# Optimization experiments

Measured on AMD Instinct MI355X. Metric: run time of the kernel, lower is better.

Reference implementation:

```python
import jax, jax.numpy as jnp
import numpy as np

B, S, H, F, E, K = 8, 4096, 256, 512, 16, 2
EPS = 1e-5


def setup_inputs() -> dict:
    key = jax.random.key(0)
    ks = jax.random.split(key, 9)
    sc = 0.02
    return {
        "x": jax.random.normal(ks[0], (B, S, H), dtype=jnp.float32),
        "gate_w": jax.random.normal(ks[1], (H, E), dtype=jnp.float32) * sc,
        "gate_b": jnp.zeros((E,), dtype=jnp.float32),
        "w1": jax.random.normal(ks[2], (E, H, F), dtype=jnp.float32) * sc,
        "b1": jnp.zeros((E, F), dtype=jnp.float32),
        "w2": jax.random.normal(ks[3], (E, F, H), dtype=jnp.float32) * sc,
        "b2": jnp.zeros((E, H), dtype=jnp.float32),
        "gamma": jnp.ones((H,), dtype=jnp.float32),
        "beta": jnp.zeros((H,), dtype=jnp.float32),
    }


def reference(x, gate_w, gate_b, w1, b1, w2, b2, gamma, beta):
    # gating: top-k over expert logits, softmax over the k selected logits
    gate_logits = x @ gate_w + gate_b                      # [B,S,E]
    topk_vals, topk_idx = jax.lax.top_k(gate_logits, K)    # [B,S,K]
    topk_w = jax.nn.softmax(topk_vals, axis=-1)            # [B,S,K]

    # naive dense MoE: every expert runs over every token (matches source)
    h = jax.nn.relu(jnp.einsum('bsh,ehf->bsef', x, w1) + b1)   # [B,S,E,F]
    expert_out = jnp.einsum('bsef,efh->bseh', h, w2) + b2       # [B,S,E,H]

    # select top-k expert outputs and combine with gate weights
    sel = jnp.take_along_axis(expert_out, topk_idx[:, :, :, None], axis=2)  # [B,S,K,H]
    moe = jnp.sum(topk_w[..., None] * sel, axis=2)              # [B,S,H]

    # residual + LayerNorm
    y = x + moe
    mu = jnp.mean(y, axis=-1, keepdims=True)
    var = jnp.var(y, axis=-1, keepdims=True)
    return (y - mu) / jnp.sqrt(var + EPS) * gamma + beta
```

## Files before the change

### kernel.cpp

```cpp
#include <hip/hip_runtime.h>
#include <hip/hip_bf16.h>

typedef __bf16 bf16_t;
typedef __bf16 bf16x8 __attribute__((ext_vector_type(8)));
typedef __bf16 bf16x4 __attribute__((ext_vector_type(4)));
typedef float f32x4 __attribute__((ext_vector_type(4)));

#define NB 8
#define NS 4096
#define NH 256
#define NF 512
#define NE 16
#define NTOK (NB*NS)
#define TT 64
#define NCH 16
#define HS_STRIDE 40

__device__ __forceinline__ void load_lds16(const void* g, void* l) {
    __builtin_amdgcn_global_load_lds(
        (const __attribute__((address_space(1))) unsigned int*)g,
        (__attribute__((address_space(3))) unsigned int*)l, 16, 0, 0);
}

__global__ __launch_bounds__(256) void prep_kernel(
    const float* __restrict__ w1, const float* __restrict__ w2,
    bf16_t* __restrict__ w1t, bf16_t* __restrict__ w2t,
    const float* __restrict__ x, const float* __restrict__ gate_w,
    const float* __restrict__ gate_b,
    int* __restrict__ counts, int* __restrict__ bucket_enc,
    float* __restrict__ bucket_gw, bf16_t* __restrict__ xb)
{
    __shared__ float tile[32][33];
    __shared__ int lcnt[NE];
    __shared__ int gbase[NE];

    if (blockIdx.x < 128) {
        if (threadIdx.x < NE) lcnt[threadIdx.x] = 0;
        __syncthreads();

        int tok = blockIdx.x * 256 + threadIdx.x;
        const float4* xr = (const float4*)(x + (size_t)tok * NH);
        bf16x4* xbr = (bf16x4*)(xb + (size_t)tok * NH);
        float acc[NE];
        #pragma unroll
        for (int e = 0; e < NE; e++) acc[e] = gate_b[e];
        for (int h4 = 0; h4 < NH / 4; h4++) {
            float4 xv = xr[h4];
            bf16x4 xo;
            xo[0] = (bf16_t)xv.x; xo[1] = (bf16_t)xv.y;
            xo[2] = (bf16_t)xv.z; xo[3] = (bf16_t)xv.w;
            xbr[h4] = xo;
            #pragma unroll
            for (int j = 0; j < 4; j++) {
                float xs = (j == 0) ? xv.x : (j == 1) ? xv.y : (j == 2) ? xv.z : xv.w;
                const float* wr = gate_w + (h4 * 4 + j) * NE;
                #pragma unroll
                for (int e = 0; e < NE; e++) acc[e] += xs * wr[e];
            }
        }
        float v0 = -1e30f, v1 = -1e30f; int i0 = 0, i1 = 0;
        #pragma unroll
        for (int e = 0; e < NE; e++) {
            float a = acc[e];
            if (a > v0)      { v1 = v0; i1 = i0; v0 = a; i0 = e; }
            else if (a > v1) { v1 = a; i1 = e; }
        }
        float e1 = __expf(v1 - v0);
        float s  = 1.f + e1;
        int   pe[2] = { i0, i1 };
        float pg[2] = { 1.f / s, e1 / s };
        int   po[2];
        po[0] = atomicAdd(&lcnt[i0], 1);
        po[1] = atomicAdd(&lcnt[i1], 1);
        __syncthreads();
        if (threadIdx.x < NE)
            gbase[threadIdx.x] = atomicAdd(&counts[threadIdx.x], lcnt[threadIdx.x]);
        __syncthreads();
        #pragma unroll
        for (int k = 0; k < 2; k++) {
            int e = pe[k];
            int pos = gbase[e] + po[k];
            bucket_enc[e * NTOK + pos] = tok | (k << 20);
            bucket_gw [e * NTOK + pos] = pg[k];
        }
        return;
    }

    int bid = blockIdx.x - 128;
    const float* src; bf16_t* dst; int R, C; int isw1;
    if (bid < 2048) { src = w1; dst = w1t; R = NH; C = NF; isw1 = 1; }
    else            { bid -= 2048; src = w2; dst = w2t; R = NF; C = NH; isw1 = 0; }
    int e = bid >> 7;
    int t = bid & 127;
    int tcols = C / 32;
    int tr = (t / tcols) * 32, tc = (t % tcols) * 32;
    src += (size_t)e * R * C;
    dst += (size_t)e * R * C;
    int tx = threadIdx.x & 31, ty0 = threadIdx.x >> 5;
    #pragma unroll
    for (int i = 0; i < 4; i++) {
        int ty = ty0 + i * 8;
        tile[ty][tx] = src[(size_t)(tr + ty) * C + tc + tx];
    }
    __syncthreads();
    if (threadIdx.x < 128) {
        int j = threadIdx.x & 31;
        int g = threadIdx.x >> 5;
        bf16x8 v;
        #pragma unroll
        for (int jj = 0; jj < 8; jj++)
            v[jj] = (bf16_t)tile[g * 8 + jj][j];
        size_t idx;
        if (isw1) {
            int f  = tc + j;
            int kb = tr + g * 8;
            idx = (size_t)f * NH + ((((kb >> 3) ^ (f & 7))) << 3);
        } else {
            int h  = tc + j;
            int fb = tr + g * 8;
            idx = ((size_t)(fb >> 5) * NH + h) * 32 + (fb & 31);
        }
        *(bf16x8*)(dst + idx) = v;
    }
}

__global__ __launch_bounds__(256, 3) void moe_kernel(
    const bf16_t* __restrict__ xb,
    const bf16_t* __restrict__ w1t,
    const float*  __restrict__ b1,
    const bf16_t* __restrict__ w2t,
    const float*  __restrict__ b2,
    const int* __restrict__ counts,
    const int* __restrict__ bucket_enc,
    const float* __restrict__ bucket_gw,
    bf16_t* __restrict__ pairbuf)
{
    __shared__ uint4 W1s4[2][1024];
    __shared__ __align__(16) bf16_t Hs[2][TT][HS_STRIDE];
    __shared__ int   tok_s[TT];
    __shared__ float gw_s[TT];
    __shared__ float b1_s[NF];
    __shared__ float b2_s[NH];

    int flat = blockIdx.x;
    int xcd  = flat & 7;
    int j    = flat >> 3;
    int e    = xcd * 2 + (j & 1);
    int tile0 = j >> 1;
    int n_e = counts[e];
    int wave = threadIdx.x >> 6;
    int lane = threadIdx.x & 63;
    int l15 = lane & 15, q = lane >> 4;

    const bf16_t* w1te = w1t + (size_t)e * NF * NH;
    const bf16_t* w2te = w2t + (size_t)e * NF * NH;

    if (threadIdx.x < 256) {
        b1_s[threadIdx.x]       = b1[e * NF + threadIdx.x];
        b1_s[threadIdx.x + 256] = b1[e * NF + threadIdx.x + 256];
        b2_s[threadIdx.x]       = b2[e * NH + threadIdx.x];
    }

    int ntiles = (n_e + TT - 1) / TT;
    for (int tile = tile0; tile < ntiles; tile += 48) {
        int tstart = tile * TT;
        __syncthreads();
        if (threadIdx.x < TT) {
            int slot = tstart + threadIdx.x;
            if (slot < n_e) {
                tok_s[threadIdx.x] = bucket_enc[e * NTOK + slot];
                gw_s [threadIdx.x] = bucket_gw [e * NTOK + slot];
            } else { tok_s[threadIdx.x] = 0; gw_s[threadIdx.x] = 0.f; }
        }
        __syncthreads();

        {
            const uint4* gw1 = (const uint4*)w1te;
            #pragma unroll
            for (int i = 0; i < 4; i++)
                load_lds16(gw1 + i * 256 + threadIdx.x, &W1s4[0][i * 256 + threadIdx.x]);
        }
        int mytok = tok_s[wave * 16 + l15] & 0xFFFFF;
        const uint4* xrow = (const uint4*)(xb + (size_t)mytok * NH);
        uint4 xf[8];
        #pragma unroll
        for (int ks = 0; ks < 8; ks++) xf[ks] = xrow[ks * 4 + q];
        bf16x8 bf2c[4], bf2n[4];
        #pragma unroll
        for (int nt = 0; nt < 4; nt++) {
            int hh = wave * 64 + nt * 16 + l15;
            bf2c[nt] = *(const bf16x8*)&w2te[((size_t)hh << 5) + q * 8];
        }
        __syncthreads();

        f32x4 oacc[4][4];
        #pragma unroll
        for (int a = 0; a < 4; a++)
            #pragma unroll
            for (int b = 0; b < 4; b++) { f32x4 z = {0.f,0.f,0.f,0.f}; oacc[a][b] = z; }

        for (int ch = 0; ch < NCH; ch++) {
            int buf = ch & 1;
            if (ch + 1 < NCH) {
                const uint4* gw1 = (const uint4*)w1te + (size_t)(ch + 1) * 1024;
                #pragma unroll
                for (int i = 0; i < 4; i++)
                    load_lds16(gw1 + i * 256 + threadIdx.x,
                               &W1s4[buf ^ 1][i * 256 + threadIdx.x]);
                #pragma unroll
                for (int nt = 0; nt < 4; nt++) {
                    int hh = wave * 64 + nt * 16 + l15;
                    bf2n[nt] = *(const bf16x8*)&w2te[(((size_t)(ch + 1) * NH + hh) << 5) + q * 8];
                }
                asm volatile("s_waitcnt vmcnt(12)" ::: "memory");
            } else {
                asm volatile("s_waitcnt vmcnt(4)" ::: "memory");
            }
            __builtin_amdgcn_s_barrier();
            __builtin_amdgcn_sched_barrier(0);

            f32x4 hacc[2]; { f32x4 z = {0.f,0.f,0.f,0.f}; hacc[0] = z; hacc[1] = z; }
            const bf16_t* w1s = (const bf16_t*)W1s4[buf];
            #pragma unroll
            for (int ks = 0; ks < 8; ks++) {
                bf16x8 xfrag = *(const bf16x8*)&xf[ks];
                #pragma unroll
                for (int n = 0; n < 2; n++) {
                    int fl = n * 16 + l15;
                    bf16x8 wf = *(const bf16x8*)&w1s[fl * NH + ((((ks * 4 + q) ^ (fl & 7))) << 3)];
                    hacc[n] = __builtin_amdgcn_mfma_f32_16x16x32_bf16(wf, xfrag, hacc[n], 0, 0, 0);
                }
            }
            #pragma unroll
            for (int n = 0; n < 2; n++) {
                int f0 = ch * 32 + n * 16 + q * 4;
                float4 b1v = *(const float4*)&b1_s[f0];
                bf16x4 hv;
                #pragma unroll
                for (int r = 0; r < 4; r++) {
                    float v = hacc[n][r] + ((const float*)&b1v)[r];
                    v = v > 0.f ? v : 0.f;
                    hv[r] = (bf16_t)v;
                }
                *(bf16x4*)&Hs[buf][wave * 16 + l15][n * 16 + q * 4] = hv;
            }
            asm volatile("s_waitcnt lgkmcnt(0)" ::: "memory");
            __builtin_amdgcn_s_barrier();
            __builtin_amdgcn_sched_barrier(0);

            #pragma unroll
            for (int mt = 0; mt < 4; mt++) {
                bf16x8 hf = *(const bf16x8*)&Hs[buf][mt * 16 + l15][q * 8];
                #pragma unroll
                for (int nt = 0; nt < 4; nt++) {
                    oacc[mt][nt] = __builtin_amdgcn_mfma_f32_16x16x32_bf16(bf2c[nt], hf, oacc[mt][nt], 0, 0, 0);
                }
            }
            if (ch + 1 < NCH) {
                #pragma unroll
                for (int nt = 0; nt < 4; nt++) bf2c[nt] = bf2n[nt];
            }
        }
        int nrows = n_e - tstart; if (nrows > TT) nrows = TT;
        float4 b2v[4];
        #pragma unroll
        for (int nt = 0; nt < 4; nt++)
            b2v[nt] = *(const float4*)&b2_s[wave * 64 + nt * 16 + q * 4];
        #pragma unroll
        for (int mt = 0; mt < 4; mt++) {
            int trow = mt * 16 + l15;
            int enc  = tok_s[trow];
            float gw = gw_s[trow];
            bool valid = trow < nrows;
            int tok = enc & 0xFFFFF;
            int kk  = enc >> 20;
            bf16_t* orow = pairbuf + ((size_t)(tok * 2 + kk)) * NH;
            #pragma unroll
            for (int nt = 0; nt < 4; nt++) {
                int col = wave * 64 + nt * 16 + q * 4;
                bf16x4 ov;
                #pragma unroll
                for (int r = 0; r < 4; r++)
                    ov[r] = (bf16_t)((oacc[mt][nt][r] + ((const float*)&b2v[nt])[r]) * gw);
                if (valid) *(bf16x4*)&orow[col] = ov;
            }
        }
    }
}

__global__ __launch_bounds__(256) void ln_kernel(
    const float* __restrict__ x, const bf16_t* __restrict__ pairbuf,
    const float* __restrict__ gamma, const float* __restrict__ beta,
    float* __restrict__ out)
{
    int tok  = blockIdx.x * 4 + (threadIdx.x >> 6);
    int lane = threadIdx.x & 63;
    float4 xv = *(const float4*)(x + (size_t)tok * NH + lane * 4);
    bf16x4 p0 = *(const bf16x4*)(pairbuf + (size_t)(tok * 2)     * NH + lane * 4);
    bf16x4 p1 = *(const bf16x4*)(pairbuf + (size_t)(tok * 2 + 1) * NH + lane * 4);
    float y0 = xv.x + (float)p0[0] + (float)p1[0];
    float y1 = xv.y + (float)p0[1] + (float)p1[1];
    float y2 = xv.z + (float)p0[2] + (float)p1[2];
    float y3 = xv.w + (float)p0[3] + (float)p1[3];
    float s  = y0 + y1 + y2 + y3;
    float s2 = y0 * y0 + y1 * y1 + y2 * y2 + y3 * y3;
    #pragma unroll
    for (int o = 32; o > 0; o >>= 1) {
        s  += __shfl_xor(s, o);
        s2 += __shfl_xor(s2, o);
    }
    float mu   = s * (1.f / NH);
    float var  = s2 * (1.f / NH) - mu * mu;
    float rstd = rsqrtf(var + 1e-5f);
    float4 gv = *(const float4*)(gamma + lane * 4);
    float4 bv = *(const float4*)(beta  + lane * 4);
    float4 o4;
    o4.x = (y0 - mu) * rstd * gv.x + bv.x;
    o4.y = (y1 - mu) * rstd * gv.y + bv.y;
    o4.z = (y2 - mu) * rstd * gv.z + bv.z;
    o4.w = (y3 - mu) * rstd * gv.w + bv.w;
    *(float4*)(out + (size_t)tok * NH + lane * 4) = o4;
}

extern "C" void kernel_launch(void* const* d_in, const int* in_sizes, int n_in,
                              void* d_out, int out_size, void* d_ws, size_t ws_size,
                              hipStream_t stream) {
    const float* x      = (const float*)d_in[0];
    const float* gate_w = (const float*)d_in[1];
    const float* gate_b = (const float*)d_in[2];
    const float* w1     = (const float*)d_in[3];
    const float* b1     = (const float*)d_in[4];
    const float* w2     = (const float*)d_in[5];
    const float* b2     = (const float*)d_in[6];
    const float* gamma  = (const float*)d_in[7];
    const float* beta   = (const float*)d_in[8];
    float* out = (float*)d_out;

    char* ws = (char*)d_ws;
    const size_t MB = 1024 * 1024;
    int*    counts     = (int*)ws;
    int*    bucket_enc = (int*)(ws + 256);
    float*  bucket_gw  = (float*)(ws + 256 + 2 * MB);
    bf16_t* w1t        = (bf16_t*)(ws + 256 + 4 * MB);
    bf16_t* w2t        = (bf16_t*)(ws + 256 + 8 * MB);
    bf16_t* xb         = (bf16_t*)(ws + 256 + 12 * MB);
    bf16_t* pairbuf    = (bf16_t*)(ws + 256 + 28 * MB);

    hipMemsetAsync(counts, 0, 256, stream);
    prep_kernel<<<4224, 256, 0, stream>>>(w1, w2, w1t, w2t,
                                          x, gate_w, gate_b,
                                          counts, bucket_enc, bucket_gw, xb);
    moe_kernel<<<768, 256, 0, stream>>>(xb, w1t, b1, w2t, b2, counts, bucket_enc, bucket_gw, pairbuf);
    ln_kernel<<<NTOK / 4, 256, 0, stream>>>(x, pairbuf, gamma, beta, out);
}
```

Before: 233.2 us.

## Add atomic per-XCD work queue and software-pipeline GEMM1/GEMM2 with triple-buffered H

Replaces the static expert/tile assignment with a per-XCD atomic work counter, so blocks on an XCD dynamically pull tiles from that XCD's two experts and load imbalance from uneven expert counts shrinks. The chunk loop is restructured so GEMM1 for chunk ch runs before GEMM2 for chunk ch-1, with H held in a triple buffer, leaving one barrier per chunk instead of two. Risks include atomic contention, re-reading the biases for every tile, and larger LDS use that could lower occupancy. The memset covers bytes 0-255, so the work counter at offset 128 is reset.

Result: no change. 236.0 us (+1.2%).

```diff
diff --git a/kernel.cpp b/kernel.cpp
--- a/kernel.cpp
+++ b/kernel.cpp
@@ -133,38 +133,40 @@
     const int* __restrict__ counts,
     const int* __restrict__ bucket_enc,
     const float* __restrict__ bucket_gw,
-    bf16_t* __restrict__ pairbuf)
+    bf16_t* __restrict__ pairbuf,
+    int* __restrict__ work_ctr)
 {
     __shared__ uint4 W1s4[2][1024];
-    __shared__ __align__(16) bf16_t Hs[2][TT][HS_STRIDE];
+    __shared__ __align__(16) bf16_t Hs[3][TT][HS_STRIDE];
     __shared__ int   tok_s[TT];
     __shared__ float gw_s[TT];
     __shared__ float b1_s[NF];
     __shared__ float b2_s[NH];
-
-    int flat = blockIdx.x;
-    int xcd  = flat & 7;
-    int j    = flat >> 3;
-    int e    = xcd * 2 + (j & 1);
-    int tile0 = j >> 1;
-    int n_e = counts[e];
+    __shared__ int   witem_s;
+
+    int xcd  = blockIdx.x & 7;
+    int e0   = xcd * 2;
     int wave = threadIdx.x >> 6;
     int lane = threadIdx.x & 63;
     int l15 = lane & 15, q = lane >> 4;
 
-    const bf16_t* w1te = w1t + (size_t)e * NF * NH;
-    const bf16_t* w2te = w2t + (size_t)e * NF * NH;
-
-    if (threadIdx.x < 256) {
-        b1_s[threadIdx.x]       = b1[e * NF + threadIdx.x];
-        b1_s[threadIdx.x + 256] = b1[e * NF + threadIdx.x + 256];
-        b2_s[threadIdx.x]       = b2[e * NH + threadIdx.x];
-    }
-
-    int ntiles = (n_e + TT - 1) / TT;
-    for (int tile = tile0; tile < ntiles; tile += 48) {
+    int n0 = counts[e0], n1 = counts[e0 + 1];
+    int nt0 = (n0 + TT - 1) / TT;
+    int Tpair = nt0 + (n1 + TT - 1) / TT;
+
+    while (true) {
+        if (threadIdx.x == 0) witem_s = atomicAdd(&work_ctr[xcd], 1);
+        __syncthreads();
+        int w = witem_s;
+        if (w >= Tpair) break;
+        int e, tile, n_e;
+        if (w < nt0) { e = e0;     tile = w;       n_e = n0; }
+        else         { e = e0 + 1; tile = w - nt0; n_e = n1; }
+
+        const bf16_t* w1te = w1t + (size_t)e * NF * NH;
+        const bf16_t* w2te = w2t + (size_t)e * NF * NH;
         int tstart = tile * TT;
-        __syncthreads();
+
         if (threadIdx.x < TT) {
             int slot = tstart + threadIdx.x;
             if (slot < n_e) {
@@ -172,6 +174,9 @@
                 gw_s [threadIdx.x] = bucket_gw [e * NTOK + slot];
             } else { tok_s[threadIdx.x] = 0; gw_s[threadIdx.x] = 0.f; }
         }
+        b1_s[threadIdx.x]       = b1[e * NF + threadIdx.x];
+        b1_s[threadIdx.x + 256] = b1[e * NF + threadIdx.x + 256];
+        b2_s[threadIdx.x]       = b2[e * NH + threadIdx.x];
         __syncthreads();
 
         {
@@ -179,6 +184,10 @@
             #pragma unroll
             for (int i = 0; i < 4; i++)
                 load_lds16(gw1 + i * 256 + threadIdx.x, &W1s4[0][i * 256 + threadIdx.x]);
+            gw1 += 1024;
+            #pragma unroll
+            for (int i = 0; i < 4; i++)
+                load_lds16(gw1 + i * 256 + threadIdx.x, &W1s4[1][i * 256 + threadIdx.x]);
         }
         int mytok = tok_s[wave * 16 + l15] & 0xFFFFF;
         const uint4* xrow = (const uint4*)(xb + (size_t)mytok * NH);
@@ -199,28 +208,9 @@
             #pragma unroll
             for (int b = 0; b < 4; b++) { f32x4 z = {0.f,0.f,0.f,0.f}; oacc[a][b] = z; }
 
-        for (int ch = 0; ch < NCH; ch++) {
-            int buf = ch & 1;
-            if (ch + 1 < NCH) {
-                const uint4* gw1 = (const uint4*)w1te + (size_t)(ch + 1) * 1024;
-                #pragma unroll
-                for (int i = 0; i < 4; i++)
-                    load_lds16(gw1 + i * 256 + threadIdx.x,
-                               &W1s4[buf ^ 1][i * 256 + threadIdx.x]);
-                #pragma unroll
-                for (int nt = 0; nt < 4; nt++) {
-                    int hh = wave * 64 + nt * 16 + l15;
-                    bf2n[nt] = *(const bf16x8*)&w2te[(((size_t)(ch + 1) * NH + hh) << 5) + q * 8];
-                }
-                asm volatile("s_waitcnt vmcnt(12)" ::: "memory");
-            } else {
-                asm volatile("s_waitcnt vmcnt(4)" ::: "memory");
-            }
-            __builtin_amdgcn_s_barrier();
-            __builtin_amdgcn_sched_barrier(0);
-
+        auto gemm1 = [&](int ch, int wbuf, int hw) {
             f32x4 hacc[2]; { f32x4 z = {0.f,0.f,0.f,0.f}; hacc[0] = z; hacc[1] = z; }
-            const bf16_t* w1s = (const bf16_t*)W1s4[buf];
+            const bf16_t* w1s = (const bf16_t*)W1s4[wbuf];
             #pragma unroll
             for (int ks = 0; ks < 8; ks++) {
                 bf16x8 xfrag = *(const bf16x8*)&xf[ks];
@@ -242,25 +232,51 @@
                     v = v > 0.f ? v : 0.f;
                     hv[r] = (bf16_t)v;
                 }
-                *(bf16x4*)&Hs[buf][wave * 16 + l15][n * 16 + q * 4] = hv;
-            }
-            asm volatile("s_waitcnt lgkmcnt(0)" ::: "memory");
-            __builtin_amdgcn_s_barrier();
-            __builtin_amdgcn_sched_barrier(0);
-
+                *(bf16x4*)&Hs[hw][wave * 16 + l15][n * 16 + q * 4] = hv;
+            }
+        };
+        auto gemm2 = [&](int hr) {
             #pragma unroll
             for (int mt = 0; mt < 4; mt++) {
-                bf16x8 hf = *(const bf16x8*)&Hs[buf][mt * 16 + l15][q * 8];
+                bf16x8 hf = *(const bf16x8*)&Hs[hr][mt * 16 + l15][q * 8];
                 #pragma unroll
                 for (int nt = 0; nt < 4; nt++) {
                     oacc[mt][nt] = __builtin_amdgcn_mfma_f32_16x16x32_bf16(bf2c[nt], hf, oacc[mt][nt], 0, 0, 0);
                 }
             }
+        };
+
+        gemm1(0, 0, 0);
+        asm volatile("s_waitcnt lgkmcnt(0)" ::: "memory");
+        __builtin_amdgcn_s_barrier();
+        __builtin_amdgcn_sched_barrier(0);
+
+        int hw = 1, hr = 0;
+        for (int ch = 1; ch < NCH; ch++) {
             if (ch + 1 < NCH) {
-                #pragma unroll
-                for (int nt = 0; nt < 4; nt++) bf2c[nt] = bf2n[nt];
-            }
-        }
+                const uint4* gw1 = (const uint4*)w1te + (size_t)(ch + 1) * 1024;
+                #pragma unroll
+                for (int i = 0; i < 4; i++)
+                    load_lds16(gw1 + i * 256 + threadIdx.x,
+                               &W1s4[(ch + 1) & 1][i * 256 + threadIdx.x]);
+            }
+            #pragma unroll
+            for (int nt = 0; nt < 4; nt++) {
+                int hh = wave * 64 + nt * 16 + l15;
+                bf2n[nt] = *(const bf16x8*)&w2te[(((size_t)ch * NH + hh) << 5) + q * 8];
+            }
+            gemm1(ch, ch & 1, hw);
+            asm volatile("s_waitcnt vmcnt(4) lgkmcnt(0)" ::: "memory");
+            __builtin_amdgcn_s_barrier();
+            __builtin_amdgcn_sched_barrier(0);
+            gemm2(hr);
+            #pragma unroll
+            for (int nt = 0; nt < 4; nt++) bf2c[nt] = bf2n[nt];
+            hw = (hw == 2) ? 0 : hw + 1;
+            hr = (hr == 2) ? 0 : hr + 1;
+        }
+        gemm2((NCH - 1) % 3);
+
         int nrows = n_e - tstart; if (nrows > TT) nrows = TT;
         float4 b2v[4];
         #pragma unroll
@@ -339,6 +355,7 @@
     char* ws = (char*)d_ws;
     const size_t MB = 1024 * 1024;
     int*    counts     = (int*)ws;
+    int*    work_ctr   = (int*)(ws + 128);
     int*    bucket_enc = (int*)(ws + 256);
     float*  bucket_gw  = (float*)(ws + 256 + 2 * MB);
     bf16_t* w1t        = (bf16_t*)(ws + 256 + 4 * MB);
@@ -350,6 +367,7 @@
     prep_kernel<<<4224, 256, 0, stream>>>(w1, w2, w1t, w2t,
                                           x, gate_w, gate_b,
                                           counts, bucket_enc, bucket_gw, xb);
-    moe_kernel<<<768, 256, 0, stream>>>(xb, w1t, b1, w2t, b2, counts, bucket_enc, bucket_gw, pairbuf);
+    moe_kernel<<<768, 256, 0, stream>>>(xb, w1t, b1, w2t, b2, counts,
+                                        bucket_enc, bucket_gw, pairbuf, work_ctr);
     ln_kernel<<<NTOK / 4, 256, 0, stream>>>(x, pairbuf, gamma, beta, out);
 }
```
